# Performance work log

Measured on AMD Instinct MI355X. Metric: run time of the kernel, lower is better.

## Reference

```python
import jax, jax.numpy as jnp
import numpy as np

M, N, H, C = 50000, 50000, 32, 128
K, GROUPS = 15, 8
CPG = C // GROUPS           # 16, channels per group
RADIUS, SIGMA, INF = 2.5, 1.0, 1.0e6
EPS = 1e-5                  # GroupNorm eps
NEG_SLOPE = 0.1             # LeakyReLU slope in alpha MLP


def setup_inputs() -> dict:
    key = jax.random.key(0)
    ks = jax.random.split(key, 12)
    q_pts = jax.random.normal(ks[0], (M, 3), jnp.float32) * 5.0
    s_pts = q_pts  # same-resolution layer: q == s
    s_feats = jax.random.normal(ks[1], (N, C), jnp.float32)
    neighb_inds = jax.random.randint(ks[2], (M, H), 0, N + 1)  # N = padding index
    # kernel points: center + 14 points in a sphere of given radius
    kp = jax.random.normal(ks[3], (K, 3), jnp.float32)
    kp = kp / (jnp.linalg.norm(kp, axis=1, keepdims=True) + 1e-9) * RADIUS * 0.66
    k_pts = kp.at[0].set(0.0)
    # alpha MLP: Linear(C->C) + LeakyReLU + Linear(C->K*CPG)
    W1 = jax.random.normal(ks[4], (C, C), jnp.float32) * np.sqrt(2.0 / C)
    b1 = jnp.zeros((C,), jnp.float32)
    W2 = jax.random.normal(ks[5], (C, K * CPG), jnp.float32) * np.sqrt(2.0 / C)
    b2 = jnp.zeros((K * CPG,), jnp.float32)
    gn_w = jnp.ones((K * CPG,), jnp.float32)
    gn_b = jnp.zeros((K * CPG,), jnp.float32)
    return {"q_pts": q_pts, "s_pts": s_pts, "s_feats": s_feats,
            "neighb_inds": neighb_inds, "k_pts": k_pts,
            "W1": W1, "b1": b1, "W2": W2, "b2": b2,
            "gn_w": gn_w, "gn_b": gn_b}


def reference(q_pts, s_pts, s_feats, k_pts, W1, b1, W2, b2, gn_w, gn_b, neighb_inds):
    m = q_pts.shape[0]
    # ---- neighbor geometry (no_grad in original) ----
    s_pts_pad = jnp.concatenate([s_pts, jnp.full((1, 3), INF, s_pts.dtype)], 0)
    neighbors = s_pts_pad[neighb_inds] - q_pts[:, None, :]          # (M,H,3)
    sq = jnp.sum((neighbors[:, :, None, :] - k_pts) ** 2, -1)       # (M,H,K)
    nn_sq = jnp.min(sq, -1)                                         # (M,H)
    nn_1nn = jnp.argmin(sq, -1)                                     # (M,H)
    infl = jnp.clip(1.0 - jnp.sqrt(nn_sq) / SIGMA, 0.0)             # linear influence
    # ---- neighbor features gather (padding row = zeros) ----
    feats_pad = jnp.concatenate([s_feats, jnp.zeros((1, C), s_feats.dtype)], 0)
    neighbor_feats = feats_pad[neighb_inds]                         # (M,H,C)
    # ---- dynamic weights from center features (q==s -> pooled = s_feats) ----
    pooled = s_feats
    h = pooled @ W1 + b1
    h = jnp.where(h >= 0, h, NEG_SLOPE * h)                         # LeakyReLU(0.1)
    cw = (h @ W2 + b2).reshape(m, K, CPG)                           # (M,K,CPG)
    # GroupNorm(K groups over K*CPG channels), stats over (points, CPG) per group
    mu = jnp.mean(cw, axis=(0, 2), keepdims=True)
    var = jnp.var(cw, axis=(0, 2), keepdims=True)
    cw = (cw - mu) * jax.lax.rsqrt(var + EPS)
    cw = cw * gn_w.reshape(1, K, CPG) + gn_b.reshape(1, K, CPG)
    # ---- gather weights at nearest kernel point, modulate by influence ----
    nw = jnp.take_along_axis(cw, nn_1nn[:, :, None], axis=1)        # (M,H,CPG)
    nw = nw * infl[:, :, None]                                      # weight_act = identity
    # ---- multiply and sum over neighbors ----
    nf = neighbor_feats.reshape(m, H, CPG, GROUPS)
    out = jnp.sum(nf * nw[:, :, :, None], axis=1)                   # (M,CPG,GROUPS)
    return out.reshape(m, C)
```

## Files before the change

kernel.cpp:

```cpp
#include <hip/hip_runtime.h>
#include <hip/hip_bf16.h>

#define Mpts 50000
#define Npts 50000
#define Hn 32
#define Cc 128
#define Kk 15
#define NCW 240

typedef __attribute__((ext_vector_type(8))) short short8;
typedef __attribute__((ext_vector_type(4))) float f32x4;
typedef __attribute__((ext_vector_type(2))) float f32x2;
typedef unsigned int u32;

__device__ inline ushort f2bf(float f) {
  __hip_bfloat16 h = __float2bfloat16(f);
  return *reinterpret_cast<ushort*>(&h);
}

__global__ __launch_bounds__(256) void k0_pre(
    const float* __restrict__ W1, const float* __restrict__ W2,
    ushort* __restrict__ sfb, ushort* __restrict__ W1t,
    ushort* __restrict__ W2t, float* __restrict__ stats)
{
  __shared__ ushort TT[240][66];
  const int t = threadIdx.x;
  const int b = blockIdx.x;
  if (b < 2) {
    const int k0 = b * 64;
#pragma unroll
    for (int i = 0; i < 32; ++i) {
      int e = t + i * 256;
      int r = e >> 7, c = e & 127;
      TT[c][r] = f2bf(W1[(size_t)(k0 + r) * Cc + c]);
    }
    __syncthreads();
    int n = t >> 1, half = t & 1;
    union { short8 v[4]; ushort u[32]; } pk;
#pragma unroll
    for (int i = 0; i < 32; ++i) pk.u[i] = TT[n][half * 32 + i];
#pragma unroll
    for (int q = 0; q < 4; ++q)
      *(short8*)(W1t + (size_t)n * Cc + k0 + half * 32 + q * 8) = pk.v[q];
  } else if (b < 4) {
    const int k0 = (b - 2) * 64;
    for (int i = 0; i < 60; ++i) {
      int e = t + i * 256;
      int r = e / 240, c = e % 240;
      TT[c][r] = f2bf(W2[(size_t)(k0 + r) * NCW + c]);
    }
    __syncthreads();
    if (t < 240) {
      union { short8 v[8]; ushort u[64]; } pk;
#pragma unroll
      for (int i = 0; i < 64; ++i) pk.u[i] = TT[t][i];
#pragma unroll
      for (int q = 0; q < 8; ++q)
        *(short8*)(W2t + (size_t)t * Cc + k0 + q * 8) = pk.v[q];
    }
  } else {
    if (t < 16) {
      short8 z = short8{0,0,0,0,0,0,0,0};
      *(short8*)(sfb + (size_t)Npts * Cc + t * 8) = z;
    }
    if (t < 128) {
      float4 z4 = make_float4(0.f, 0.f, 0.f, 0.f);
      *(float4*)(stats + t * 4) = z4;
    }
  }
}

__global__ __launch_bounds__(256, 3) void k1_mlp(
    const float* __restrict__ sfeat, const ushort* __restrict__ W1t,
    const float* __restrict__ b1, const ushort* __restrict__ W2t,
    const float* __restrict__ b2, ushort* __restrict__ sfb,
    ushort* __restrict__ cw, float* __restrict__ stats,
    const float* __restrict__ q_pts, const float* __restrict__ s_pts,
    const int* __restrict__ nb, const float* __restrict__ kp,
    u32* __restrict__ geomP)
{
  __shared__ __align__(16) ushort shA[64 * 128];
  __shared__ __align__(16) ushort shW[128 * 128];
  __shared__ float red[2][15][4];
  __shared__ float kptS[45];

  const int t = threadIdx.x;
  const int r0 = blockIdx.x * 64;
  const int wid = t >> 6, lane = t & 63;
  const int l16 = lane & 15, lq = lane >> 4;

  if (t < 45) kptS[t] = kp[t];

  float4 fA[4], fB[4];
#pragma unroll
  for (int p = 0; p < 4; ++p) {
    int id = p * 256 + t;
    int r = id >> 4, c = id & 15;
    int g = r0 + r;
    fA[p] = make_float4(0.f, 0.f, 0.f, 0.f);
    fB[p] = make_float4(0.f, 0.f, 0.f, 0.f);
    if (g < Mpts) {
      const float* src = sfeat + (size_t)g * Cc + c * 8;
      fA[p] = *(const float4*)(src);
      fB[p] = *(const float4*)(src + 4);
    }
  }
  uint4 wv[8];
#pragma unroll
  for (int p = 0; p < 8; ++p) {
    int id = p * 256 + t;
    int r = id >> 4, c = id & 15;
    wv[p] = *(const uint4*)(W1t + r * Cc + c * 8);
  }
  asm volatile("" :: "v"(wv[0].x), "v"(wv[1].x), "v"(wv[2].x), "v"(wv[3].x),
                     "v"(wv[4].x), "v"(wv[5].x), "v"(wv[6].x), "v"(wv[7].x),
                     "v"(fA[0].x), "v"(fA[1].x), "v"(fA[2].x), "v"(fA[3].x),
                     "v"(fB[0].x), "v"(fB[1].x), "v"(fB[2].x), "v"(fB[3].x));
#pragma unroll
  for (int p = 0; p < 8; ++p) {
    int id = p * 256 + t;
    int r = id >> 4, c = id & 15;
    *(uint4*)((char*)shW + ((r * 256 + c * 16) ^ ((r & 7) << 4))) = wv[p];
  }
#pragma unroll
  for (int p = 0; p < 4; ++p) {
    int id = p * 256 + t;
    int r = id >> 4, c = id & 15;
    int g = r0 + r;
    union { short8 s; ushort u[8]; } pk;
    pk.u[0] = f2bf(fA[p].x); pk.u[1] = f2bf(fA[p].y); pk.u[2] = f2bf(fA[p].z); pk.u[3] = f2bf(fA[p].w);
    pk.u[4] = f2bf(fB[p].x); pk.u[5] = f2bf(fB[p].y); pk.u[6] = f2bf(fB[p].z); pk.u[7] = f2bf(fB[p].w);
    if (g < Mpts) *(short8*)(sfb + (size_t)g * Cc + c * 8) = pk.s;
    *(short8*)((char*)shA + ((r * 256 + c * 16) ^ ((r & 7) << 4))) = pk.s;
  }
  __syncthreads();

  const int arow = wid * 16 + l16;
  const int axor = (arow & 7) << 4;

  f32x4 acc1[8];
#pragma unroll
  for (int nt = 0; nt < 8; ++nt) acc1[nt] = f32x4{0.f, 0.f, 0.f, 0.f};
#pragma unroll
  for (int kt = 0; kt < 4; ++kt) {
    const int koff2 = (kt * 32 + lq * 8) * 2;
    short8 a = *(const short8*)((const char*)shA + ((arow * 256 + koff2) ^ axor));
#pragma unroll
    for (int nt = 0; nt < 8; ++nt) {
      int wrow = nt * 16 + l16;
      short8 b = *(const short8*)((const char*)shW + ((wrow * 256 + koff2) ^ ((wrow & 7) << 4)));
      acc1[nt] = __builtin_amdgcn_mfma_f32_16x16x32_bf16(a, b, acc1[nt], 0, 0, 0);
    }
  }
#pragma unroll
  for (int nt = 0; nt < 8; ++nt) {
    int col = nt * 16 + l16;
    float bias = b1[col];
#pragma unroll
    for (int reg = 0; reg < 4; ++reg) {
      float h = acc1[nt][reg] + bias;
      h = h >= 0.f ? h : 0.1f * h;
      int row = wid * 16 + lq * 4 + reg;
      int byte = ((row * 256) + col * 2) ^ ((row & 7) << 4);
      *(ushort*)((char*)shA + byte) = f2bf(h);
    }
  }

  f32x4 acc2[8], acc3[7];
#pragma unroll
  for (int j = 0; j < 8; ++j) acc2[j] = f32x4{0.f, 0.f, 0.f, 0.f};
#pragma unroll
  for (int j = 0; j < 7; ++j) acc3[j] = f32x4{0.f, 0.f, 0.f, 0.f};

  __syncthreads();
  {
    uint4 wv2[8];
#pragma unroll
    for (int p = 0; p < 8; ++p) {
      int id = p * 256 + t;
      int r = id >> 4, c = id & 15;
      wv2[p] = *(const uint4*)(W2t + (size_t)r * Cc + c * 8);
    }
    asm volatile("" :: "v"(wv2[0].x), "v"(wv2[1].x), "v"(wv2[2].x), "v"(wv2[3].x),
                       "v"(wv2[4].x), "v"(wv2[5].x), "v"(wv2[6].x), "v"(wv2[7].x));
#pragma unroll
    for (int p = 0; p < 8; ++p) {
      int id = p * 256 + t;
      int r = id >> 4, c = id & 15;
      *(uint4*)((char*)shW + ((r * 256 + c * 16) ^ ((r & 7) << 4))) = wv2[p];
    }
  }
  __syncthreads();
#pragma unroll
  for (int kt = 0; kt < 4; ++kt) {
    const int koff2 = (kt * 32 + lq * 8) * 2;
    short8 a = *(const short8*)((const char*)shA + ((arow * 256 + koff2) ^ axor));
#pragma unroll
    for (int j = 0; j < 8; ++j) {
      int wrow = j * 16 + l16;
      short8 b = *(const short8*)((const char*)shW + ((wrow * 256 + koff2) ^ ((wrow & 7) << 4)));
      acc2[j] = __builtin_amdgcn_mfma_f32_16x16x32_bf16(a, b, acc2[j], 0, 0, 0);
    }
  }

  __syncthreads();
  {
    uint4 wv2[7];
#pragma unroll
    for (int p = 0; p < 7; ++p) {
      int id = p * 256 + t;
      int r = id >> 4, c = id & 15;
      wv2[p] = *(const uint4*)(W2t + (size_t)(128 + r) * Cc + c * 8);
    }
    asm volatile("" :: "v"(wv2[0].x), "v"(wv2[1].x), "v"(wv2[2].x), "v"(wv2[3].x),
                       "v"(wv2[4].x), "v"(wv2[5].x), "v"(wv2[6].x));
#pragma unroll
    for (int p = 0; p < 7; ++p) {
      int id = p * 256 + t;
      int r = id >> 4, c = id & 15;
      *(uint4*)((char*)shW + ((r * 256 + c * 16) ^ ((r & 7) << 4))) = wv2[p];
    }
  }
  __syncthreads();
#pragma unroll
  for (int kt = 0; kt < 4; ++kt) {
    const int koff2 = (kt * 32 + lq * 8) * 2;
    short8 a = *(const short8*)((const char*)shA + ((arow * 256 + koff2) ^ axor));
#pragma unroll
    for (int j = 0; j < 7; ++j) {
      int wrow = j * 16 + l16;
      short8 b = *(const short8*)((const char*)shW + ((wrow * 256 + koff2) ^ ((wrow & 7) << 4)));
      acc3[j] = __builtin_amdgcn_mfma_f32_16x16x32_bf16(a, b, acc3[j], 0, 0, 0);
    }
  }
  __syncthreads();

  ushort* shB = shW;
  float s[15], ss[15];
#pragma unroll
  for (int j = 0; j < 15; ++j) { s[j] = 0.f; ss[j] = 0.f; }
  const int rowb = wid * 16 + lq * 4;
#pragma unroll
  for (int j = 0; j < 15; ++j) {
    int col = j * 16 + l16;
    float bias = b2[col];
#pragma unroll
    for (int reg = 0; reg < 4; ++reg) {
      float v = (j < 8 ? acc2[j][reg] : acc3[j - 8][reg]) + bias;
      shB[(rowb + reg) * 244 + col] = f2bf(v);
      if (r0 + rowb + reg < Mpts) { s[j] += v; ss[j] += v * v; }
    }
  }
  __syncthreads();

  {
    char* cwB = (char*)cw + (size_t)r0 * 480;
#pragma unroll
    for (int i = 0; i < 8; ++i) {
      int gid = i * 256 + t;
      if (gid < 1920) {
        int row = gid / 30;
        int rem = (gid - row * 30) * 16;
        if (r0 + row < Mpts) {
          uint4 v = *(const uint4*)((const char*)shB + row * 488 + rem);
          *(uint4*)(cwB + (size_t)row * 480 + rem) = v;
        }
      }
    }
  }

  {
    const int gbase = blockIdx.x * 2048 + t;
#pragma unroll
    for (int i = 0; i < 8; ++i) {
      int gt = gbase + i * 256;
      if (gt < Mpts * Hn) {
        int idx = nb[gt]; if (idx > Npts) idx = Npts;
        int m = gt >> 5;
        float qx = q_pts[m * 3 + 0], qy = q_pts[m * 3 + 1], qz = q_pts[m * 3 + 2];
        float px, py, pz;
        if (idx < Npts) { px = s_pts[idx * 3 + 0]; py = s_pts[idx * 3 + 1]; pz = s_pts[idx * 3 + 2]; }
        else            { px = 1.0e6f; py = 1.0e6f; pz = 1.0e6f; }
        float nx = px - qx, ny = py - qy, nz = pz - qz;
        int ksel = 0; float best = 1e30f;
#pragma unroll
        for (int k = 0; k < Kk; ++k) {
          float dx = nx - kptS[k * 3 + 0], dy = ny - kptS[k * 3 + 1], dz = nz - kptS[k * 3 + 2];
          float d = dx * dx + dy * dy + dz * dz;
          if (d < best) { best = d; ksel = k; }
        }
        float infl = 1.f - sqrtf(best);
        infl = infl > 0.f ? infl : 0.f;
        geomP[gt] = (__float_as_uint(infl) & 0xFFFFFFF0u) | (u32)ksel;
      }
    }
  }

#pragma unroll
  for (int j = 0; j < 15; ++j) {
    for (int off = 32; off > 0; off >>= 1) {
      s[j]  += __shfl_xor(s[j],  off);
      ss[j] += __shfl_xor(ss[j], off);
    }
  }
  if (lane == 0) {
#pragma unroll
    for (int j = 0; j < 15; ++j) { red[0][j][wid] = s[j]; red[1][j][wid] = ss[j]; }
  }
  __syncthreads();
  float* st = stats + (blockIdx.x & 7) * 64;
  if (t < 15) {
    float S = red[0][t][0] + red[0][t][1] + red[0][t][2] + red[0][t][3];
    atomicAdd(&st[t], S);
  } else if (t >= 32 && t < 47) {
    int j = t - 32;
    float SS = red[1][j][0] + red[1][j][1] + red[1][j][2] + red[1][j][3];
    atomicAdd(&st[32 + j], SS);
  }
}

__global__ __launch_bounds__(256) void k3_out(
    const ushort* __restrict__ sfb, const int* __restrict__ nb,
    const u32* __restrict__ geomP, const float* __restrict__ gn_w,
    const float* __restrict__ gn_b, const float* __restrict__ stats,
    const ushort* __restrict__ cw, float* __restrict__ out)
{
  __shared__ float Atab[255], Btab[255];
  __shared__ float mus[16], rss[16];
  __shared__ float wtab[4][2][8][33];
  const int t = threadIdx.x;

  if (t < 15) {
    float S = 0.f, SS = 0.f;
#pragma unroll
    for (int r = 0; r < 8; ++r) { S += stats[r * 64 + t]; SS += stats[r * 64 + 32 + t]; }
    const float inv = 1.0f / (16.0f * (float)Mpts);
    float mu = S * inv;
    float var = SS * inv - mu * mu;
    mus[t] = mu;
    rss[t] = rsqrtf(var + 1e-5f);
  }
  __syncthreads();
  if (t < 240) {
    int k = t >> 4, c = t & 15;
    float a = rss[k] * gn_w[t];
    Atab[k * 17 + c] = a;
    Btab[k * 17 + c] = gn_b[t] - mus[k] * a;
  }
  __syncthreads();

  const int half = (blockIdx.x >= 6250) ? 1 : 0;
  const int pblk = blockIdx.x - half * 6250;
  const int wid = t >> 6, lane = t & 63;
  const int mbase = pblk * 8 + wid * 2;
  const int gtid = pblk * 256 + t;
  const int ch = lane & 7, hlane = (lane >> 3) & 3, p = lane >> 5;
  const int half8 = half * 8;

  u32 g = geomP[gtid];
  int idxv = nb[gtid]; if (idxv > Npts) idxv = Npts;

  const uint4* fb = (const uint4*)sfb;
  uint4 fv[8];
#pragma unroll
  for (int j = 0; j < 8; ++j) {
    int ih = __shfl(idxv, (p << 5) | (hlane + 4 * j));
    fv[j] = fb[ih * 16 + half8 + ch];
  }

  {
    int h = lane >> 1, c0 = (lane & 1) * 4;
#pragma unroll
    for (int q = 0; q < 2; ++q) {
      u32 gp = __shfl((int)g, (q << 5) | h);
      int kh = gp & 15;
      float wI = __uint_as_float(gp & 0xFFFFFFF0u);
      uint2 cwv = *(const uint2*)(cw + (size_t)(mbase + q) * NCW + kh * 16 + half8 + c0);
      const float* Ar = &Atab[kh * 17 + half8 + c0];
      const float* Br = &Btab[kh * 17 + half8 + c0];
      float v0 = __uint_as_float(cwv.x << 16);
      float v1 = __uint_as_float(cwv.x & 0xffff0000u);
      float v2 = __uint_as_float(cwv.y << 16);
      float v3 = __uint_as_float(cwv.y & 0xffff0000u);
      wtab[wid][q][c0 + 0][h] = fmaf(v0, Ar[0], Br[0]) * wI;
      wtab[wid][q][c0 + 1][h] = fmaf(v1, Ar[1], Br[1]) * wI;
      wtab[wid][q][c0 + 2][h] = fmaf(v2, Ar[2], Br[2]) * wI;
      wtab[wid][q][c0 + 3][h] = fmaf(v3, Ar[3], Br[3]) * wI;
    }
  }

  asm volatile("" :: "v"(fv[0].x), "v"(fv[1].x), "v"(fv[2].x), "v"(fv[3].x),
                     "v"(fv[4].x), "v"(fv[5].x), "v"(fv[6].x), "v"(fv[7].x));

  f32x2 a0 = {0.f, 0.f}, a1 = {0.f, 0.f}, a2 = {0.f, 0.f}, a3 = {0.f, 0.f};
#pragma unroll
  for (int j = 0; j < 8; ++j) {
    float w = wtab[wid][p][ch][hlane + 4 * j];
    f32x2 w2 = {w, w};
    u32 ux = fv[j].x, uy = fv[j].y, uz = fv[j].z, uw = fv[j].w;
    f32x2 q0 = {__uint_as_float(ux << 16), __uint_as_float(ux & 0xffff0000u)};
    f32x2 q1 = {__uint_as_float(uy << 16), __uint_as_float(uy & 0xffff0000u)};
    f32x2 q2 = {__uint_as_float(uz << 16), __uint_as_float(uz & 0xffff0000u)};
    f32x2 q3 = {__uint_as_float(uw << 16), __uint_as_float(uw & 0xffff0000u)};
    a0 = __builtin_elementwise_fma(q0, w2, a0);
    a1 = __builtin_elementwise_fma(q1, w2, a1);
    a2 = __builtin_elementwise_fma(q2, w2, a2);
    a3 = __builtin_elementwise_fma(q3, w2, a3);
  }
#pragma unroll
  for (int off = 8; off <= 16; off <<= 1) {
    a0[0] += __shfl_xor(a0[0], off); a0[1] += __shfl_xor(a0[1], off);
    a1[0] += __shfl_xor(a1[0], off); a1[1] += __shfl_xor(a1[1], off);
    a2[0] += __shfl_xor(a2[0], off); a2[1] += __shfl_xor(a2[1], off);
    a3[0] += __shfl_xor(a3[0], off); a3[1] += __shfl_xor(a3[1], off);
  }
  if ((lane & 24) == 0) {
    float* op = out + (size_t)(mbase + p) * Cc + half * 64 + ch * 8;
    float4 o0; o0.x = a0[0]; o0.y = a0[1]; o0.z = a1[0]; o0.w = a1[1];
    float4 o1; o1.x = a2[0]; o1.y = a2[1]; o1.z = a3[0]; o1.w = a3[1];
    *(float4*)(op)     = o0;
    *(float4*)(op + 4) = o1;
  }
}

extern "C" void kernel_launch(void* const* d_in, const int* in_sizes, int n_in,
                              void* d_out, int out_size, void* d_ws, size_t ws_size,
                              hipStream_t stream) {
  const float* q_pts  = (const float*)d_in[0];
  const float* s_pts  = (const float*)d_in[1];
  const float* sfeat  = (const float*)d_in[2];
  const int*   nb     = (const int*)d_in[3];
  const float* kp     = (const float*)d_in[4];
  const float* W1     = (const float*)d_in[5];
  const float* b1     = (const float*)d_in[6];
  const float* W2     = (const float*)d_in[7];
  const float* b2     = (const float*)d_in[8];
  const float* gn_w   = (const float*)d_in[9];
  const float* gn_b   = (const float*)d_in[10];
  float* out   = (float*)d_out;

  char* wsb = (char*)d_ws;
  float*  stats = (float*)wsb;
  ushort* sfb   = (ushort*)(wsb + 4096);
  ushort* W1t   = (ushort*)(wsb + 12804352);
  ushort* W2t   = (ushort*)(wsb + 12837120);
  ushort* cwb   = (ushort*)(wsb + 12898560);
  u32*    geomP = (u32*)   (wsb + 36898560);

  k0_pre<<<5, 256, 0, stream>>>(W1, W2, sfb, W1t, W2t, stats);
  k1_mlp<<<(Mpts + 63) / 64, 256, 0, stream>>>(sfeat, W1t, b1, W2t, b2,
                                               sfb, cwb, stats,
                                               q_pts, s_pts, nb, kp, geomP);
  k3_out<<<12500, 256, 0, stream>>>(sfb, nb, geomP, gn_w, gn_b, stats,
                                    cwb, out);
}
```

Baseline: 105.1 us.

## Split bf16 feature table into half-channel planes and move geometry into separate blocks

The bf16 copy of the source features is stored as two separate 64-channel planes (low and high halves), so each k3_out half-pass gathers from a compact 128-byte-row table rather than strided halves of 256-byte rows. This is meant to improve cache-line locality for the random neighbour gathers. The per-neighbour nearest-kernel-point geometry is also moved out of the MLP blocks into 6250 extra lightweight blocks of the same launch. Those blocks no longer carry the heavy LDS and register footprint of the matmul blocks while doing gather work. The cost is a larger grid with early-return blocks and a second buffer pointer to manage.

After: 93.94 us (median of 2 runs). 10.6% less time.

```diff
diff --git a/kernel.cpp b/kernel.cpp
--- a/kernel.cpp
+++ b/kernel.cpp
@@ -7,6 +7,7 @@
 #define Cc 128
 #define Kk 15
 #define NCW 240
+#define NBLK1 782
 
 typedef __attribute__((ext_vector_type(8))) short short8;
 typedef __attribute__((ext_vector_type(4))) float f32x4;
@@ -20,8 +21,9 @@
 
 __global__ __launch_bounds__(256) void k0_pre(
     const float* __restrict__ W1, const float* __restrict__ W2,
-    ushort* __restrict__ sfb, ushort* __restrict__ W1t,
-    ushort* __restrict__ W2t, float* __restrict__ stats)
+    ushort* __restrict__ sfbL, ushort* __restrict__ sfbH,
+    ushort* __restrict__ W1t, ushort* __restrict__ W2t,
+    float* __restrict__ stats)
 {
   __shared__ ushort TT[240][66];
   const int t = threadIdx.x;
@@ -59,10 +61,9 @@
         *(short8*)(W2t + (size_t)t * Cc + k0 + q * 8) = pk.v[q];
     }
   } else {
-    if (t < 16) {
-      short8 z = short8{0,0,0,0,0,0,0,0};
-      *(short8*)(sfb + (size_t)Npts * Cc + t * 8) = z;
-    }
+    short8 z = short8{0,0,0,0,0,0,0,0};
+    if (t < 8)                  *(short8*)(sfbL + (size_t)Npts * 64 + t * 8) = z;
+    else if (t < 16)            *(short8*)(sfbH + (size_t)Npts * 64 + (t - 8) * 8) = z;
     if (t < 128) {
       float4 z4 = make_float4(0.f, 0.f, 0.f, 0.f);
       *(float4*)(stats + t * 4) = z4;
@@ -70,11 +71,12 @@
   }
 }
 
-__global__ __launch_bounds__(256, 3) void k1_mlp(
+__global__ __launch_bounds__(256, 3) void k1_mix(
     const float* __restrict__ sfeat, const ushort* __restrict__ W1t,
     const float* __restrict__ b1, const ushort* __restrict__ W2t,
-    const float* __restrict__ b2, ushort* __restrict__ sfb,
-    ushort* __restrict__ cw, float* __restrict__ stats,
+    const float* __restrict__ b2, ushort* __restrict__ sfbL,
+    ushort* __restrict__ sfbH, ushort* __restrict__ cw,
+    float* __restrict__ stats,
     const float* __restrict__ q_pts, const float* __restrict__ s_pts,
     const int* __restrict__ nb, const float* __restrict__ kp,
     u32* __restrict__ geomP)
@@ -85,11 +87,34 @@
   __shared__ float kptS[45];
 
   const int t = threadIdx.x;
+
+  if (blockIdx.x >= NBLK1) {
+    if (t < 45) kptS[t] = kp[t];
+    __syncthreads();
+    const int gtid = (blockIdx.x - NBLK1) * 256 + t;
+    const int m = gtid >> 5;
+    int idx = nb[gtid]; if (idx > Npts) idx = Npts;
+    float qx = q_pts[m * 3 + 0], qy = q_pts[m * 3 + 1], qz = q_pts[m * 3 + 2];
+    float px, py, pz;
+    if (idx < Npts) { px = s_pts[idx * 3 + 0]; py = s_pts[idx * 3 + 1]; pz = s_pts[idx * 3 + 2]; }
+    else            { px = 1.0e6f; py = 1.0e6f; pz = 1.0e6f; }
+    float nx = px - qx, ny = py - qy, nz = pz - qz;
+    int ksel = 0; float best = 1e30f;
+#pragma unroll
+    for (int k = 0; k < Kk; ++k) {
+      float dx = nx - kptS[k * 3 + 0], dy = ny - kptS[k * 3 + 1], dz = nz - kptS[k * 3 + 2];
+      float d = dx * dx + dy * dy + dz * dz;
+      if (d < best) { best = d; ksel = k; }
+    }
+    float infl = 1.f - sqrtf(best);
+    infl = infl > 0.f ? infl : 0.f;
+    geomP[gtid] = (__float_as_uint(infl) & 0xFFFFFFF0u) | (u32)ksel;
+    return;
+  }
+
   const int r0 = blockIdx.x * 64;
   const int wid = t >> 6, lane = t & 63;
   const int l16 = lane & 15, lq = lane >> 4;
-
-  if (t < 45) kptS[t] = kp[t];
 
   float4 fA[4], fB[4];
 #pragma unroll
@@ -130,7 +155,10 @@
     union { short8 s; ushort u[8]; } pk;
     pk.u[0] = f2bf(fA[p].x); pk.u[1] = f2bf(fA[p].y); pk.u[2] = f2bf(fA[p].z); pk.u[3] = f2bf(fA[p].w);
     pk.u[4] = f2bf(fB[p].x); pk.u[5] = f2bf(fB[p].y); pk.u[6] = f2bf(fB[p].z); pk.u[7] = f2bf(fB[p].w);
-    if (g < Mpts) *(short8*)(sfb + (size_t)g * Cc + c * 8) = pk.s;
+    if (g < Mpts) {
+      ushort* dst = (c < 8 ? sfbL : sfbH) + (size_t)g * 64 + (c & 7) * 8;
+      *(short8*)dst = pk.s;
+    }
     *(short8*)((char*)shA + ((r * 256 + c * 16) ^ ((r & 7) << 4))) = pk.s;
   }
   __syncthreads();
@@ -269,33 +297,6 @@
     }
   }
 
-  {
-    const int gbase = blockIdx.x * 2048 + t;
-#pragma unroll
-    for (int i = 0; i < 8; ++i) {
-      int gt = gbase + i * 256;
-      if (gt < Mpts * Hn) {
-        int idx = nb[gt]; if (idx > Npts) idx = Npts;
-        int m = gt >> 5;
-        float qx = q_pts[m * 3 + 0], qy = q_pts[m * 3 + 1], qz = q_pts[m * 3 + 2];
-        float px, py, pz;
-        if (idx < Npts) { px = s_pts[idx * 3 + 0]; py = s_pts[idx * 3 + 1]; pz = s_pts[idx * 3 + 2]; }
-        else            { px = 1.0e6f; py = 1.0e6f; pz = 1.0e6f; }
-        float nx = px - qx, ny = py - qy, nz = pz - qz;
-        int ksel = 0; float best = 1e30f;
-#pragma unroll
-        for (int k = 0; k < Kk; ++k) {
-          float dx = nx - kptS[k * 3 + 0], dy = ny - kptS[k * 3 + 1], dz = nz - kptS[k * 3 + 2];
-          float d = dx * dx + dy * dy + dz * dz;
-          if (d < best) { best = d; ksel = k; }
-        }
-        float infl = 1.f - sqrtf(best);
-        infl = infl > 0.f ? infl : 0.f;
-        geomP[gt] = (__float_as_uint(infl) & 0xFFFFFFF0u) | (u32)ksel;
-      }
-    }
-  }
-
 #pragma unroll
   for (int j = 0; j < 15; ++j) {
     for (int off = 32; off > 0; off >>= 1) {
@@ -320,10 +321,11 @@
 }
 
 __global__ __launch_bounds__(256) void k3_out(
-    const ushort* __restrict__ sfb, const int* __restrict__ nb,
-    const u32* __restrict__ geomP, const float* __restrict__ gn_w,
-    const float* __restrict__ gn_b, const float* __restrict__ stats,
-    const ushort* __restrict__ cw, float* __restrict__ out)
+    const ushort* __restrict__ sfbL, const ushort* __restrict__ sfbH,
+    const int* __restrict__ nb, const u32* __restrict__ geomP,
+    const float* __restrict__ gn_w, const float* __restrict__ gn_b,
+    const float* __restrict__ stats, const ushort* __restrict__ cw,
+    float* __restrict__ out)
 {
   __shared__ float Atab[255], Btab[255];
   __shared__ float mus[16], rss[16];
@@ -360,12 +362,12 @@
   u32 g = geomP[gtid];
   int idxv = nb[gtid]; if (idxv > Npts) idxv = Npts;
 
-  const uint4* fb = (const uint4*)sfb;
+  const uint4* fb = (const uint4*)(half ? sfbH : sfbL);
   uint4 fv[8];
 #pragma unroll
   for (int j = 0; j < 8; ++j) {
     int ih = __shfl(idxv, (p << 5) | (hlane + 4 * j));
-    fv[j] = fb[ih * 16 + half8 + ch];
+    fv[j] = fb[ih * 8 + ch];
   }
 
   {
@@ -441,16 +443,17 @@
 
   char* wsb = (char*)d_ws;
   float*  stats = (float*)wsb;
-  ushort* sfb   = (ushort*)(wsb + 4096);
+  ushort* sfbL  = (ushort*)(wsb + 4096);
+  ushort* sfbH  = (ushort*)(wsb + 6404224);
   ushort* W1t   = (ushort*)(wsb + 12804352);
   ushort* W2t   = (ushort*)(wsb + 12837120);
   ushort* cwb   = (ushort*)(wsb + 12898560);
   u32*    geomP = (u32*)   (wsb + 36898560);
 
-  k0_pre<<<5, 256, 0, stream>>>(W1, W2, sfb, W1t, W2t, stats);
-  k1_mlp<<<(Mpts + 63) / 64, 256, 0, stream>>>(sfeat, W1t, b1, W2t, b2,
-                                               sfb, cwb, stats,
-                                               q_pts, s_pts, nb, kp, geomP);
-  k3_out<<<12500, 256, 0, stream>>>(sfb, nb, geomP, gn_w, gn_b, stats,
-                                    cwb, out);
+  k0_pre<<<5, 256, 0, stream>>>(W1, W2, sfbL, sfbH, W1t, W2t, stats);
+  k1_mix<<<NBLK1 + 6250, 256, 0, stream>>>(sfeat, W1t, b1, W2t, b2,
+                                           sfbL, sfbH, cwb, stats,
+                                           q_pts, s_pts, nb, kp, geomP);
+  k3_out<<<12500, 256, 0, stream>>>(sfbL, sfbH, nb, geomP, gn_w, gn_b,
+                                    stats, cwb, out);
 }
```
